# Optimization experiments

Measured on AMD Instinct MI355X. Metric: run time of the kernel, lower is better.

## Reference

```python
import jax, jax.numpy as jnp
import numpy as np

N_NODES = 100000
BN_EPS = 1e-5


def _cheb_bn_prelu(x, src, dst, w, W, b, a, g, be):
    # ChebConv K=3 with sym normalization, lambda_max=2 => L_hat = -D^-1/2 A D^-1/2
    def lap(v):
        return jax.ops.segment_sum(w[:, None] * v[src], dst, num_segments=N_NODES)
    Tx1 = lap(x)                      # [N, F]
    Tx2 = 2.0 * lap(Tx1) - x
    out = x @ W[0] + Tx1 @ W[1] + Tx2 @ W[2] + b
    out = jnp.where(out > 0, out, a * out)          # PReLU (single param)
    mu = out.mean(0)
    var = out.var(0)                                 # biased, as torch BN
    return (out - mu) / jnp.sqrt(var + BN_EPS) * g + be


def setup_inputs() -> dict:
    key = jax.random.key(0)
    ks = jax.random.split(key, 40)
    N, E, H = N_NODES, 3200000, 64
    inp = {
        'x': jax.random.normal(ks[0], (N, 3), jnp.float32),
        'pos': jax.random.normal(ks[1], (N, 3), jnp.float32),
        'normals': jax.random.normal(ks[2], (N, 3), jnp.float32),
        'edge_index': jax.random.randint(ks[3], (2, E), 0, N, jnp.int64 if jax.config.read('jax_enable_x64') else jnp.int32),
    }
    dims = [(9, H), (H, H), (H, H), (H, H // 2)]
    i = 4
    for m, (fi, fo) in enumerate(dims, start=1):
        s = 1.0 / np.sqrt(fi)
        inp[f'W{m}'] = jax.random.uniform(ks[i], (3, fi, fo), jnp.float32, -s, s); i += 1
        inp[f'b{m}'] = jax.random.uniform(ks[i], (fo,), jnp.float32, -s, s); i += 1
        inp[f'a{m}'] = jnp.full((1,), 0.25, jnp.float32)
        inp[f'g{m}'] = jnp.ones((fo,), jnp.float32)
        inp[f'be{m}'] = jnp.zeros((fo,), jnp.float32)
    hh = H // 2
    for m in range(1, 4):
        s = 1.0 / np.sqrt(hh)
        inp[f'h{m}w'] = jax.random.uniform(ks[i], (hh, hh), jnp.float32, -s, s); i += 1
        inp[f'h{m}b'] = jax.random.uniform(ks[i], (hh,), jnp.float32, -s, s); i += 1
    return inp


def reference(x, pos, normals, edge_index,
              W1, b1, a1, g1, be1, W2, b2, a2, g2, be2,
              W3, b3, a3, g3, be3, W4, b4, a4, g4, be4,
              h1w, h1b, h2w, h2b, h3w, h3b):
    src, dst = edge_index[0], edge_index[1]
    deg = jax.ops.segment_sum(jnp.ones(src.shape[0], x.dtype), src, num_segments=N_NODES)
    dis = jnp.where(deg > 0, jax.lax.rsqrt(jnp.maximum(deg, 1.0)), 0.0)
    w = -dis[src] * dis[dst]                         # scaled Laplacian edge weights
    h = jnp.concatenate([x, pos, normals], axis=1)   # [N, 9]
    h = _cheb_bn_prelu(h, src, dst, w, W1, b1, a1, g1, be1)
    h = _cheb_bn_prelu(h, src, dst, w, W2, b2, a2, g2, be2)
    h = _cheb_bn_prelu(h, src, dst, w, W3, b3, a3, g3, be3)
    h = _cheb_bn_prelu(h, src, dst, w, W4, b4, a4, g4, be4)
    h = jax.nn.relu(h @ h1w + h1b)
    h = jax.nn.relu(h @ h2w + h2b)
    return h @ h3w + h3b                              # [N, 32] logits
```

## Files before the change

kernel.cpp:

```cpp
#include <hip/hip_runtime.h>

constexpr float BN_EPS = 1e-5f;
constexpr int HB = 256;

__device__ __forceinline__ float bf2f(unsigned short u) {
  return __uint_as_float(((unsigned)u) << 16);
}
__device__ __forceinline__ unsigned short f2bf(float f) {
  union { float f; unsigned u; } v; v.f = f;
  unsigned r = v.u + 0x7FFF + ((v.u >> 16) & 1);
  return (unsigned short)(r >> 16);
}


__global__ void __launch_bounds__(1024) hist_lds_kernel(const int* __restrict__ keys, int E, int slice,
                                                        unsigned* __restrict__ partials, int NW) {
  extern __shared__ unsigned lds[];
  int tid = threadIdx.x, b = blockIdx.x;
  for (int w = tid; w < NW; w += 1024) lds[w] = 0;
  __syncthreads();
  int e0 = b * slice, e1 = e0 + slice; if (e1 > E) e1 = E;
  for (int e = e0 + tid; e < e1; e += 1024) {
    int n = keys[e];
    atomicAdd(&lds[n >> 2], 1u << (8 * (n & 3)));
  }
  __syncthreads();
  unsigned* out = partials + (size_t)b * NW;
  for (int w = tid; w < NW; w += 1024) out[w] = lds[w];
}

__global__ void combine_kernel(unsigned* __restrict__ pA, const unsigned* __restrict__ pB,
                               float* __restrict__ dis, int* __restrict__ cnt, int NW, int N) {
  int w = blockIdx.x * blockDim.x + threadIdx.x;
  if (w >= NW) return;
  unsigned sumA = 0;
  for (int b = 0; b < HB; ++b) sumA += pA[(size_t)b * NW + w];
  unsigned runB = 0;
  for (int b = 0; b < HB; ++b) {
    unsigned v = pB[(size_t)b * NW + w];
    pA[(size_t)b * NW + w] = runB;
    runB += v;
  }
  int n0 = w * 4;
#pragma unroll
  for (int j = 0; j < 4; ++j) {
    int n = n0 + j;
    if (n < N) {
      unsigned da = (sumA >> (8 * j)) & 255u;
      unsigned db = (runB >> (8 * j)) & 255u;
      dis[n] = da > 0 ? rsqrtf((float)da) : 0.f;
      cnt[n] = (int)db;
    }
  }
}

__global__ void scan1_kernel(const int* __restrict__ cnt, int N,
                             int* __restrict__ rowptr, int* __restrict__ bsums) {
  int tid = threadIdx.x, lane = tid & 63, wid = tid >> 6;
  int i = blockIdx.x * 256 + tid;
  int v = (i < N) ? cnt[i] : 0;
  int incl = v;
#pragma unroll
  for (int off = 1; off < 64; off <<= 1) {
    int u = __shfl_up(incl, off);
    if (lane >= off) incl += u;
  }
  __shared__ int wt[4];
  if (lane == 63) wt[wid] = incl;
  __syncthreads();
  int woff = 0;
  for (int w = 0; w < wid; ++w) woff += wt[w];
  if (i < N) rowptr[i] = woff + incl - v;
  if (tid == 255) bsums[blockIdx.x] = woff + incl;
}

__global__ void scan2_kernel(int* __restrict__ bsums, int NB, int* __restrict__ rowptr, int N) {
  int tid = threadIdx.x, lane = tid & 63, wid = tid >> 6;
  int v = (tid < NB) ? bsums[tid] : 0;
  int incl = v;
#pragma unroll
  for (int off = 1; off < 64; off <<= 1) {
    int u = __shfl_up(incl, off);
    if (lane >= off) incl += u;
  }
  __shared__ int wt[16];
  if (lane == 63) wt[wid] = incl;
  __syncthreads();
  int woff = 0;
  for (int w = 0; w < wid; ++w) woff += wt[w];
  if (tid < NB) bsums[tid] = woff + incl - v;
  if (tid == blockDim.x - 1) rowptr[N] = woff + incl;
}

__global__ void scan3_kernel(int* __restrict__ rowptr, const int* __restrict__ bsums, int N) {
  int i = blockIdx.x * 256 + threadIdx.x;
  if (i < N) rowptr[i] += bsums[blockIdx.x];
}

__global__ void __launch_bounds__(1024) scatter2_kernel(
    const int* __restrict__ src, const int* __restrict__ dst, int E, int slice,
    const unsigned* __restrict__ baseTbl, int NW, const int* __restrict__ rowptr,
    const float* __restrict__ dis, int2* __restrict__ pk) {
  extern __shared__ unsigned lds[];
  int tid = threadIdx.x, b = blockIdx.x;
  const unsigned* base = baseTbl + (size_t)b * NW;
  for (int w = tid; w < NW; w += 1024) lds[w] = base[w];
  __syncthreads();
  int e0 = b * slice, e1 = e0 + slice; if (e1 > E) e1 = E;
  for (int e = e0 + tid; e < e1; e += 1024) {
    int s = src[e], d = dst[e];
    unsigned prev = atomicAdd(&lds[d >> 2], 1u << (8 * (d & 3)));
    int p = rowptr[d] + (int)((prev >> (8 * (d & 3))) & 255u);
    pk[p] = make_int2(s, __float_as_int(-dis[s] * dis[d]));
  }
}

__global__ void pack_kernel(const float* __restrict__ x, const float* __restrict__ pos,
                            const float* __restrict__ nrm, ushort* __restrict__ h0b, int N) {
  int idx = blockIdx.x * blockDim.x + threadIdx.x;
  if (idx < N * 16) {
    int n = idx >> 4, c = idx & 15;
    float v = 0.f;
    if (c < 3) v = x[n * 3 + c];
    else if (c < 6) v = pos[n * 3 + c - 3];
    else if (c < 9) v = nrm[n * 3 + c - 6];
    h0b[idx] = f2bf(v);
  }
}


template <bool AFFINE>
__global__ __launch_bounds__(256) void lap64_kernel(
    const ushort4* __restrict__ vb, ushort4* __restrict__ outb,
    const int* __restrict__ rowptr, const int2* __restrict__ pk,
    const float* __restrict__ st, int N) {
  int tid = threadIdx.x, lane = tid & 63, wid = tid >> 6;
  int node = blockIdx.x * 4 + wid;
  if (node >= N) return;
  int g = lane >> 4, q = lane & 15;
  int r0 = rowptr[node], r1 = rowptr[node + 1];
  float4 a = {0.f, 0.f, 0.f, 0.f}, b = {0.f, 0.f, 0.f, 0.f};
  float ws = 0.f, ws2 = 0.f;
  int k = r0 + g;
  for (; k + 12 < r1; k += 16) {
    int2 p0 = pk[k], p1 = pk[k + 4], p2 = pk[k + 8], p3 = pk[k + 12];
    ushort4 u0 = vb[(size_t)p0.x * 16 + q];
    ushort4 u1 = vb[(size_t)p1.x * 16 + q];
    ushort4 u2 = vb[(size_t)p2.x * 16 + q];
    ushort4 u3 = vb[(size_t)p3.x * 16 + q];
    float w0 = __int_as_float(p0.y), w1 = __int_as_float(p1.y);
    float w2 = __int_as_float(p2.y), w3 = __int_as_float(p3.y);
    ws += w0 + w2; ws2 += w1 + w3;
    a.x = fmaf(w0, bf2f(u0.x), a.x); a.y = fmaf(w0, bf2f(u0.y), a.y);
    a.z = fmaf(w0, bf2f(u0.z), a.z); a.w = fmaf(w0, bf2f(u0.w), a.w);
    b.x = fmaf(w1, bf2f(u1.x), b.x); b.y = fmaf(w1, bf2f(u1.y), b.y);
    b.z = fmaf(w1, bf2f(u1.z), b.z); b.w = fmaf(w1, bf2f(u1.w), b.w);
    a.x = fmaf(w2, bf2f(u2.x), a.x); a.y = fmaf(w2, bf2f(u2.y), a.y);
    a.z = fmaf(w2, bf2f(u2.z), a.z); a.w = fmaf(w2, bf2f(u2.w), a.w);
    b.x = fmaf(w3, bf2f(u3.x), b.x); b.y = fmaf(w3, bf2f(u3.y), b.y);
    b.z = fmaf(w3, bf2f(u3.z), b.z); b.w = fmaf(w3, bf2f(u3.w), b.w);
  }
  for (; k < r1; k += 4) {
    int2 p0 = pk[k];
    ushort4 u0 = vb[(size_t)p0.x * 16 + q];
    float w0 = __int_as_float(p0.y);
    ws += w0;
    a.x = fmaf(w0, bf2f(u0.x), a.x); a.y = fmaf(w0, bf2f(u0.y), a.y);
    a.z = fmaf(w0, bf2f(u0.z), a.z); a.w = fmaf(w0, bf2f(u0.w), a.w);
  }
  a.x += b.x; a.y += b.y; a.z += b.z; a.w += b.w; ws += ws2;
  a.x += __shfl_xor(a.x, 16); a.y += __shfl_xor(a.y, 16);
  a.z += __shfl_xor(a.z, 16); a.w += __shfl_xor(a.w, 16);
  ws += __shfl_xor(ws, 16);
  a.x += __shfl_xor(a.x, 32); a.y += __shfl_xor(a.y, 32);
  a.z += __shfl_xor(a.z, 32); a.w += __shfl_xor(a.w, 32);
  ws += __shfl_xor(ws, 32);
  if (g == 0) {
    float4 o = a;
    if (AFFINE) {
      float4 s4 = *(const float4*)(st + q * 4);
      float4 t4 = *(const float4*)(st + 64 + q * 4);
      o.x = fmaf(a.x, s4.x, ws * t4.x);
      o.y = fmaf(a.y, s4.y, ws * t4.y);
      o.z = fmaf(a.z, s4.z, ws * t4.z);
      o.w = fmaf(a.w, s4.w, ws * t4.w);
    }
    ushort4 ub;
    ub.x = f2bf(o.x); ub.y = f2bf(o.y); ub.z = f2bf(o.z); ub.w = f2bf(o.w);
    outb[(size_t)node * 16 + q] = ub;
  }
}


__global__ __launch_bounds__(256) void lap16_kernel(const ushort4* __restrict__ vb,
                                                    ushort4* __restrict__ outb,
                                                    const int* __restrict__ rowptr,
                                                    const int2* __restrict__ pk, int N) {
  int tid = threadIdx.x, lane = tid & 63, wid = tid >> 6;
  int node = (blockIdx.x * 4 + wid) * 4 + (lane >> 4);
  int sub = lane & 15, g = sub >> 2, q = sub & 3;
  float4 acc = {0.f, 0.f, 0.f, 0.f};
  if (node < N) {
    int r0 = rowptr[node], r1 = rowptr[node + 1];
    for (int k = r0 + g; k < r1; k += 4) {
      int2 pr = pk[k];
      float w = __int_as_float(pr.y);
      ushort4 u = vb[(size_t)pr.x * 4 + q];
      acc.x = fmaf(w, bf2f(u.x), acc.x); acc.y = fmaf(w, bf2f(u.y), acc.y);
      acc.z = fmaf(w, bf2f(u.z), acc.z); acc.w = fmaf(w, bf2f(u.w), acc.w);
    }
  }
  acc.x += __shfl_xor(acc.x, 4); acc.y += __shfl_xor(acc.y, 4);
  acc.z += __shfl_xor(acc.z, 4); acc.w += __shfl_xor(acc.w, 4);
  acc.x += __shfl_xor(acc.x, 8); acc.y += __shfl_xor(acc.y, 8);
  acc.z += __shfl_xor(acc.z, 8); acc.w += __shfl_xor(acc.w, 8);
  if (node < N && g == 0) {
    ushort4 ub;
    ub.x = f2bf(acc.x); ub.y = f2bf(acc.y); ub.z = f2bf(acc.z); ub.w = f2bf(acc.w);
    outb[(size_t)node * 4 + q] = ub;
  }
}


template <int F_IN, int F_OUT, bool NORMH>
__global__ __launch_bounds__(256) void mm_kernel(
    const ushort* hb, const ushort* t1b, const ushort* t2b,
    ushort* outb,
    const float* __restrict__ W, const float* __restrict__ bias,
    const float* __restrict__ aP, const float* __restrict__ stPrev,
    float* __restrict__ bp, int N, int f_in_real, int ntiles) {
  constexpr int CPT = F_OUT / 16;
  constexpr int WSZ = 3 * F_IN * F_OUT;
  constexpr int RSZ = 16 * F_OUT * 2;
  constexpr int SM = (WSZ > RSZ) ? WSZ : RSZ;
  __shared__ float sm[SM];
  __shared__ float smS[F_IN], smT[F_IN];

  int tid = threadIdx.x;
  const int S = f_in_real * F_OUT;
  for (int idx = tid; idx < WSZ; idx += 256) {
    int m = idx / (F_IN * F_OUT);
    int r = idx - m * (F_IN * F_OUT);
    int i = r / F_OUT, c = r - i * F_OUT;
    float v = 0.f;
    if (i < f_in_real) {
      int b = i * F_OUT + c;
      if (m == 0)      v = W[b] - W[2 * S + b];
      else if (m == 1) v = W[S + b];
      else             v = 2.f * W[2 * S + b];
    }
    sm[idx] = v;
  }
  if (NORMH && tid < F_IN) { smS[tid] = stPrev[tid]; smT[tid] = stPrev[64 + tid]; }
  __syncthreads();

  const int cg = tid & 15;
  const int ngt = tid >> 4;
  const int c0 = cg * CPT;
  const float alpha = aP[0];
  float bb[CPT];
#pragma unroll
  for (int c = 0; c < CPT; ++c) bb[c] = bias[c0 + c];

  float ssum[CPT], ssq[CPT];
#pragma unroll
  for (int c = 0; c < CPT; ++c) { ssum[c] = 0.f; ssq[c] = 0.f; }

  for (int tile = blockIdx.x; tile < ntiles; tile += gridDim.x) {
    const int node0 = tile * 64 + ngt * 4;
    float acc[4][CPT];
#pragma unroll
    for (int j = 0; j < 4; ++j)
#pragma unroll
      for (int c = 0; c < CPT; ++c) acc[j][c] = 0.f;

#pragma unroll
    for (int m = 0; m < 3; ++m) {
      const ushort* A = (m == 0 ? hb : (m == 1 ? t1b : t2b)) + (size_t)node0 * F_IN;
      const float* Bm = sm + m * F_IN * F_OUT;
#pragma unroll 2
      for (int kb = 0; kb < F_IN / 4; ++kb) {
        float ar[4][4];
#pragma unroll
        for (int j = 0; j < 4; ++j) {
          ushort4 u = *(const ushort4*)(A + j * F_IN + kb * 4);
          ar[j][0] = bf2f(u.x); ar[j][1] = bf2f(u.y);
          ar[j][2] = bf2f(u.z); ar[j][3] = bf2f(u.w);
        }
        if (NORMH && m == 0) {
          float4 sv = *(const float4*)(smS + kb * 4);
          float4 tv = *(const float4*)(smT + kb * 4);
#pragma unroll
          for (int j = 0; j < 4; ++j) {
            ar[j][0] = fmaf(ar[j][0], sv.x, tv.x);
            ar[j][1] = fmaf(ar[j][1], sv.y, tv.y);
            ar[j][2] = fmaf(ar[j][2], sv.z, tv.z);
            ar[j][3] = fmaf(ar[j][3], sv.w, tv.w);
          }
        }
#pragma unroll
        for (int kk = 0; kk < 4; ++kk) {
          const float* Brow = Bm + (kb * 4 + kk) * F_OUT + c0;
          float br[CPT];
          if constexpr (CPT == 4) *(float4*)br = *(const float4*)Brow;
          else                    *(float2*)br = *(const float2*)Brow;
#pragma unroll
          for (int j = 0; j < 4; ++j)
#pragma unroll
            for (int c = 0; c < CPT; ++c)
              acc[j][c] = fmaf(ar[j][kk], br[c], acc[j][c]);
        }
      }
    }

#pragma unroll
    for (int j = 0; j < 4; ++j) {
      int node = node0 + j;
      if (node < N) {
        float v[CPT];
#pragma unroll
        for (int c = 0; c < CPT; ++c) {
          float t = acc[j][c] + bb[c];
          t = t > 0.f ? t : alpha * t;
          v[c] = t;
          ssum[c] += t;
          ssq[c] += t * t;
        }
        ushort* o = outb + (size_t)node * 64 + c0;
        if constexpr (CPT == 4) {
          uint2 ub;
          ub.x = (unsigned)f2bf(v[0]) | ((unsigned)f2bf(v[1]) << 16);
          ub.y = (unsigned)f2bf(v[2]) | ((unsigned)f2bf(v[3]) << 16);
          *(uint2*)o = ub;
        } else {
          unsigned ub = (unsigned)f2bf(v[0]) | ((unsigned)f2bf(v[1]) << 16);
          *(unsigned*)o = ub;
        }
      }
    }
  }

  __syncthreads();
#pragma unroll
  for (int c = 0; c < CPT; ++c) {
    sm[(ngt * F_OUT + c0 + c) * 2 + 0] = ssum[c];
    sm[(ngt * F_OUT + c0 + c) * 2 + 1] = ssq[c];
  }
  __syncthreads();
  if (tid < 128) {
    int col = tid & 63, stat = tid >> 6;
    float tot = 0.f;
    if (col < F_OUT) {
#pragma unroll 8
      for (int g = 0; g < 16; ++g) tot += sm[(g * F_OUT + col) * 2 + stat];
    }
    bp[(size_t)blockIdx.x * 128 + stat * 64 + col] = tot;
  }
}


__global__ void stats_kernel(const float* __restrict__ bp, int nb,
                             const float* __restrict__ g, const float* __restrict__ be,
                             float* __restrict__ st, int F_OUT, float invN) {
  __shared__ float red[1024];
  int tid = threadIdx.x;
  int t = tid & 127, c = tid >> 7;
  float s = 0.f;
  for (int w = c; w < nb; w += 8) s += bp[(size_t)w * 128 + t];
  red[tid] = s;
  __syncthreads();
  if (tid < 128) {
    float tot = 0.f;
    for (int cc = 0; cc < 8; ++cc) tot += red[cc * 128 + tid];
    red[tid] = tot;
  }
  __syncthreads();
  if (tid < F_OUT) {
    float sum = red[tid], sq = red[64 + tid];
    float mu = sum * invN;
    float var = sq * invN - mu * mu;
    float sc = g[tid] * rsqrtf(var + BN_EPS);
    st[tid] = sc;
    st[64 + tid] = be[tid] - mu * sc;
  }
}


__global__ __launch_bounds__(256) void mlp_kernel(const ushort* __restrict__ hb,
    const float* __restrict__ st,
    const float* __restrict__ w1, const float* __restrict__ b1,
    const float* __restrict__ w2, const float* __restrict__ b2,
    const float* __restrict__ w3, const float* __restrict__ b3,
    float* __restrict__ out, int N, int ntiles) {
  __shared__ float Wl[3][1024];
  __shared__ float Bl[3][32];
  __shared__ float S4[32], T4[32];
  __shared__ float act[2][128][36];
  int tid = threadIdx.x;
  for (int idx = tid; idx < 1024; idx += 256) {
    Wl[0][idx] = w1[idx];
    Wl[1][idx] = w2[idx];
    Wl[2][idx] = w3[idx];
  }
  if (tid < 32) {
    Bl[0][tid] = b1[tid]; Bl[1][tid] = b2[tid]; Bl[2][tid] = b3[tid];
    S4[tid] = st[tid]; T4[tid] = st[64 + tid];
  }
  __syncthreads();

  const int cg = tid & 7, ng = tid >> 3;
  const int c0 = cg * 4;
  const int nl = ng * 4;

  for (int tile = blockIdx.x; tile < ntiles; tile += gridDim.x) {
    const int node0 = tile * 128 + nl;
    float acc[4][4];

#pragma unroll
    for (int j = 0; j < 4; ++j)
#pragma unroll
      for (int c = 0; c < 4; ++c) acc[j][c] = 0.f;
#pragma unroll
    for (int kb = 0; kb < 8; ++kb) {
      float ar[4][4];
#pragma unroll
      for (int j = 0; j < 4; ++j) {
        int node = node0 + j;
        if (node < N) {
          ushort4 u = *(const ushort4*)(hb + (size_t)node * 64 + kb * 4);
          ar[j][0] = fmaf(bf2f(u.x), S4[kb * 4 + 0], T4[kb * 4 + 0]);
          ar[j][1] = fmaf(bf2f(u.y), S4[kb * 4 + 1], T4[kb * 4 + 1]);
          ar[j][2] = fmaf(bf2f(u.z), S4[kb * 4 + 2], T4[kb * 4 + 2]);
          ar[j][3] = fmaf(bf2f(u.w), S4[kb * 4 + 3], T4[kb * 4 + 3]);
        } else {
          ar[j][0] = ar[j][1] = ar[j][2] = ar[j][3] = 0.f;
        }
      }
#pragma unroll
      for (int kk = 0; kk < 4; ++kk) {
        float br[4];
        *(float4*)br = *(const float4*)(&Wl[0][(kb * 4 + kk) * 32 + c0]);
#pragma unroll
        for (int j = 0; j < 4; ++j)
#pragma unroll
          for (int c = 0; c < 4; ++c)
            acc[j][c] = fmaf(ar[j][kk], br[c], acc[j][c]);
      }
    }
#pragma unroll
    for (int j = 0; j < 4; ++j) {
      float v[4];
#pragma unroll
      for (int c = 0; c < 4; ++c) v[c] = fmaxf(acc[j][c] + Bl[0][c0 + c], 0.f);
      *(float4*)(&act[0][nl + j][c0]) = *(float4*)v;
    }
    __syncthreads();

#pragma unroll
    for (int j = 0; j < 4; ++j)
#pragma unroll
      for (int c = 0; c < 4; ++c) acc[j][c] = 0.f;
#pragma unroll
    for (int kb = 0; kb < 8; ++kb) {
      float ar[4][4];
#pragma unroll
      for (int j = 0; j < 4; ++j)
        *(float4*)ar[j] = *(const float4*)(&act[0][nl + j][kb * 4]);
#pragma unroll
      for (int kk = 0; kk < 4; ++kk) {
        float br[4];
        *(float4*)br = *(const float4*)(&Wl[1][(kb * 4 + kk) * 32 + c0]);
#pragma unroll
        for (int j = 0; j < 4; ++j)
#pragma unroll
          for (int c = 0; c < 4; ++c)
            acc[j][c] = fmaf(ar[j][kk], br[c], acc[j][c]);
      }
    }
#pragma unroll
    for (int j = 0; j < 4; ++j) {
      float v[4];
#pragma unroll
      for (int c = 0; c < 4; ++c) v[c] = fmaxf(acc[j][c] + Bl[1][c0 + c], 0.f);
      *(float4*)(&act[1][nl + j][c0]) = *(float4*)v;
    }
    __syncthreads();

#pragma unroll
    for (int j = 0; j < 4; ++j)
#pragma unroll
      for (int c = 0; c < 4; ++c) acc[j][c] = 0.f;
#pragma unroll
    for (int kb = 0; kb < 8; ++kb) {
      float ar[4][4];
#pragma unroll
      for (int j = 0; j < 4; ++j)
        *(float4*)ar[j] = *(const float4*)(&act[1][nl + j][kb * 4]);
#pragma unroll
      for (int kk = 0; kk < 4; ++kk) {
        float br[4];
        *(float4*)br = *(const float4*)(&Wl[2][(kb * 4 + kk) * 32 + c0]);
#pragma unroll
        for (int j = 0; j < 4; ++j)
#pragma unroll
          for (int c = 0; c < 4; ++c)
            acc[j][c] = fmaf(ar[j][kk], br[c], acc[j][c]);
      }
    }
#pragma unroll
    for (int j = 0; j < 4; ++j) {
      int node = node0 + j;
      if (node < N) {
        float v[4];
#pragma unroll
        for (int c = 0; c < 4; ++c) v[c] = acc[j][c] + Bl[2][c0 + c];
        *(float4*)(out + (size_t)node * 32 + c0) = *(float4*)v;
      }
    }
    __syncthreads();
  }
}


extern "C" void kernel_launch(void* const* d_in, const int* in_sizes, int n_in,
                              void* d_out, int out_size, void* d_ws, size_t ws_size,
                              hipStream_t stream) {
  const float* x   = (const float*)d_in[0];
  const float* pos = (const float*)d_in[1];
  const float* nrm = (const float*)d_in[2];
  const int*   ei  = (const int*)d_in[3];
  const float* W1p = (const float*)d_in[4];
  const float* b1p = (const float*)d_in[5];
  const float* a1p = (const float*)d_in[6];
  const float* g1p = (const float*)d_in[7];
  const float* be1p= (const float*)d_in[8];
  const float* W2p = (const float*)d_in[9];
  const float* b2p = (const float*)d_in[10];
  const float* a2p = (const float*)d_in[11];
  const float* g2p = (const float*)d_in[12];
  const float* be2p= (const float*)d_in[13];
  const float* W3p = (const float*)d_in[14];
  const float* b3p = (const float*)d_in[15];
  const float* a3p = (const float*)d_in[16];
  const float* g3p = (const float*)d_in[17];
  const float* be3p= (const float*)d_in[18];
  const float* W4p = (const float*)d_in[19];
  const float* b4p = (const float*)d_in[20];
  const float* a4p = (const float*)d_in[21];
  const float* g4p = (const float*)d_in[22];
  const float* be4p= (const float*)d_in[23];
  const float* h1w = (const float*)d_in[24];
  const float* h1b = (const float*)d_in[25];
  const float* h2w = (const float*)d_in[26];
  const float* h2b = (const float*)d_in[27];
  const float* h3w = (const float*)d_in[28];
  const float* h3b = (const float*)d_in[29];

  const int N = in_sizes[0] / 3;
  const int E = in_sizes[3] / 2;
  const int* src = ei;
  const int* dst = ei + E;

  const int NW = (N + 3) / 4;
  const size_t ldsBytes = (size_t)NW * 4;
  const int slice = (E + HB - 1) / HB;

  char* p = (char*)d_ws;
  auto alloc = [&](size_t bytes) -> void* {
    void* r = (void*)p;
    p += (bytes + 255) & ~(size_t)255;
    return r;
  };
  float*    dis      = (float*)   alloc((size_t)N * 4);
  int*      rowptr   = (int*)     alloc((size_t)(N + 1) * 4);
  int*      cnt      = (int*)     alloc((size_t)N * 4);
  int*      bsums    = (int*)     alloc(4096 * 4);
  unsigned* partialsA= (unsigned*)alloc((size_t)HB * NW * 4);
  unsigned* partialsB= (unsigned*)alloc((size_t)HB * NW * 4);
  int2*     pk       = (int2*)partialsB;
  ushort*   bufHb    = (ushort*)  alloc((size_t)N * 64 * 2);
  ushort*   bufT1b   = (ushort*)  alloc((size_t)N * 64 * 2);
  ushort*   bufT2b   = (ushort*)  alloc((size_t)N * 64 * 2);
  ushort*   bufH16b  = (ushort*)  alloc((size_t)N * 16 * 2);
  ushort*   bufT116b = (ushort*)  alloc((size_t)N * 16 * 2);
  ushort*   bufT216b = (ushort*)  alloc((size_t)N * 16 * 2);
  const int MMB = 768;
  float*    bp       = (float*)   alloc((size_t)MMB * 128 * 4);
  float*    stats    = (float*)   alloc(512 * 4);
  float* st1 = stats, *st2 = stats + 128, *st3 = stats + 256, *st4 = stats + 384;

  int gN = (N + 255) / 256;
  hist_lds_kernel<<<HB, 1024, ldsBytes, stream>>>(src, E, slice, partialsA, NW);
  hist_lds_kernel<<<HB, 1024, ldsBytes, stream>>>(dst, E, slice, partialsB, NW);
  combine_kernel<<<(NW + 255) / 256, 256, 0, stream>>>(partialsA, partialsB, dis, cnt, NW, N);
  scan1_kernel<<<gN, 256, 0, stream>>>(cnt, N, rowptr, bsums);
  scan2_kernel<<<1, 1024, 0, stream>>>(bsums, gN, rowptr, N);
  scan3_kernel<<<gN, 256, 0, stream>>>(rowptr, bsums, N);
  scatter2_kernel<<<HB, 1024, ldsBytes, stream>>>(src, dst, E, slice, partialsA, NW, rowptr, dis, pk);
  pack_kernel<<<(N * 16 + 255) / 256, 256, 0, stream>>>(x, pos, nrm, bufH16b, N);

  const float invN = 1.f / (float)N;
  int g64 = (N + 3) / 4, g16 = (N + 15) / 16;
  const int ntiles = (N + 63) / 64;
  const int ntilesM = (N + 127) / 128;

  lap16_kernel<<<g16, 256, 0, stream>>>((const ushort4*)bufH16b, (ushort4*)bufT116b, rowptr, pk, N);
  lap16_kernel<<<g16, 256, 0, stream>>>((const ushort4*)bufT116b, (ushort4*)bufT216b, rowptr, pk, N);
  mm_kernel<16, 64, false><<<MMB, 256, 0, stream>>>(bufH16b, bufT116b, bufT216b, bufHb,
      W1p, b1p, a1p, nullptr, bp, N, 9, ntiles);
  stats_kernel<<<1, 1024, 0, stream>>>(bp, MMB, g1p, be1p, st1, 64, invN);

  lap64_kernel<true><<<g64, 256, 0, stream>>>((const ushort4*)bufHb, (ushort4*)bufT1b,
      rowptr, pk, st1, N);
  lap64_kernel<false><<<g64, 256, 0, stream>>>((const ushort4*)bufT1b, (ushort4*)bufT2b,
      rowptr, pk, nullptr, N);
  mm_kernel<64, 64, true><<<MMB, 256, 0, stream>>>(bufHb, bufT1b, bufT2b, bufHb,
      W2p, b2p, a2p, st1, bp, N, 64, ntiles);
  stats_kernel<<<1, 1024, 0, stream>>>(bp, MMB, g2p, be2p, st2, 64, invN);

  lap64_kernel<true><<<g64, 256, 0, stream>>>((const ushort4*)bufHb, (ushort4*)bufT1b,
      rowptr, pk, st2, N);
  lap64_kernel<false><<<g64, 256, 0, stream>>>((const ushort4*)bufT1b, (ushort4*)bufT2b,
      rowptr, pk, nullptr, N);
  mm_kernel<64, 64, true><<<MMB, 256, 0, stream>>>(bufHb, bufT1b, bufT2b, bufHb,
      W3p, b3p, a3p, st2, bp, N, 64, ntiles);
  stats_kernel<<<1, 1024, 0, stream>>>(bp, MMB, g3p, be3p, st3, 64, invN);

  lap64_kernel<true><<<g64, 256, 0, stream>>>((const ushort4*)bufHb, (ushort4*)bufT1b,
      rowptr, pk, st3, N);
  lap64_kernel<false><<<g64, 256, 0, stream>>>((const ushort4*)bufT1b, (ushort4*)bufT2b,
      rowptr, pk, nullptr, N);
  mm_kernel<64, 32, true><<<MMB, 256, 0, stream>>>(bufHb, bufT1b, bufT2b, bufHb,
      W4p, b4p, a4p, st3, bp, N, 64, ntiles);
  stats_kernel<<<1, 1024, 0, stream>>>(bp, MMB, g4p, be4p, st4, 32, invN);

  mlp_kernel<<<MMB, 256, 0, stream>>>(bufHb, st4, h1w, h1b, h2w, h2b, h3w, h3b,
      (float*)d_out, N, ntilesM);
}
```

Baseline: 908.4 us.

## Replace scalar FMA dense transforms with bf16 MFMA kernel and fold BN into weights

The per-layer dense transform (three Chebyshev terms times weight matrices) moves from scalar fp32 FMAs to 16x16x32 bf16 MFMA instructions, with weight fragments held in registers. The previous layer's batch-norm scale is folded into the weights and its shift into the bias, so the per-element normalization in the inner loop goes away. The first layer packs x, T1 and T2 into one 64-wide interleaved buffer so it runs as a single K=64 MFMA pass. Weights are now rounded to bf16, which adds precision error, and the wider first-layer buffer adds some memory traffic.

```diff
diff --git a/kernel.cpp b/kernel.cpp
--- a/kernel.cpp
+++ b/kernel.cpp
@@ -2,6 +2,9 @@
 
 constexpr float BN_EPS = 1e-5f;
 constexpr int HB = 256;
+
+using short8  = __attribute__((ext_vector_type(8))) short;
+using floatx4 = __attribute__((ext_vector_type(4))) float;
 
 __device__ __forceinline__ float bf2f(unsigned short u) {
   return __uint_as_float(((unsigned)u) << 16);
@@ -116,15 +119,15 @@
 }
 
 __global__ void pack_kernel(const float* __restrict__ x, const float* __restrict__ pos,
-                            const float* __restrict__ nrm, ushort* __restrict__ h0b, int N) {
+                            const float* __restrict__ nrm, ushort* __restrict__ h0c, int N) {
   int idx = blockIdx.x * blockDim.x + threadIdx.x;
-  if (idx < N * 16) {
-    int n = idx >> 4, c = idx & 15;
+  if (idx < N * 64) {
+    int n = idx >> 6, c = idx & 63;
     float v = 0.f;
     if (c < 3) v = x[n * 3 + c];
     else if (c < 6) v = pos[n * 3 + c - 3];
     else if (c < 9) v = nrm[n * 3 + c - 6];
-    h0b[idx] = f2bf(v);
+    h0c[idx] = f2bf(v);
   }
 }
 
@@ -195,7 +198,8 @@
 __global__ __launch_bounds__(256) void lap16_kernel(const ushort4* __restrict__ vb,
                                                     ushort4* __restrict__ outb,
                                                     const int* __restrict__ rowptr,
-                                                    const int2* __restrict__ pk, int N) {
+                                                    const int2* __restrict__ pk, int N,
+                                                    int inOff, int outOff) {
   int tid = threadIdx.x, lane = tid & 63, wid = tid >> 6;
   int node = (blockIdx.x * 4 + wid) * 4 + (lane >> 4);
   int sub = lane & 15, g = sub >> 2, q = sub & 3;
@@ -205,7 +209,7 @@
     for (int k = r0 + g; k < r1; k += 4) {
       int2 pr = pk[k];
       float w = __int_as_float(pr.y);
-      ushort4 u = vb[(size_t)pr.x * 4 + q];
+      ushort4 u = vb[(size_t)pr.x * 16 + inOff + q];
       acc.x = fmaf(w, bf2f(u.x), acc.x); acc.y = fmaf(w, bf2f(u.y), acc.y);
       acc.z = fmaf(w, bf2f(u.z), acc.z); acc.w = fmaf(w, bf2f(u.w), acc.w);
     }
@@ -217,143 +221,127 @@
   if (node < N && g == 0) {
     ushort4 ub;
     ub.x = f2bf(acc.x); ub.y = f2bf(acc.y); ub.z = f2bf(acc.z); ub.w = f2bf(acc.w);
-    outb[(size_t)node * 4 + q] = ub;
-  }
-}
-
-
-template <int F_IN, int F_OUT, bool NORMH>
-__global__ __launch_bounds__(256) void mm_kernel(
-    const ushort* hb, const ushort* t1b, const ushort* t2b,
-    ushort* outb,
+    outb[(size_t)node * 16 + outOff + q] = ub;
+  }
+}
+
+
+template <int NMAT, int F_OUT, bool NORMH>
+__global__ __launch_bounds__(256) void mmfma_kernel(
+    const ushort* __restrict__ A0, const ushort* __restrict__ A1, const ushort* __restrict__ A2,
+    ushort* __restrict__ outb,
     const float* __restrict__ W, const float* __restrict__ bias,
     const float* __restrict__ aP, const float* __restrict__ stPrev,
     float* __restrict__ bp, int N, int f_in_real, int ntiles) {
-  constexpr int CPT = F_OUT / 16;
-  constexpr int WSZ = 3 * F_IN * F_OUT;
-  constexpr int RSZ = 16 * F_OUT * 2;
-  constexpr int SM = (WSZ > RSZ) ? WSZ : RSZ;
-  __shared__ float sm[SM];
-  __shared__ float smS[F_IN], smT[F_IN];
-
+  constexpr int NFRAG = F_OUT / 16;
+  constexpr int NKF = NMAT * 2;
+  constexpr int TOTF = NKF * NFRAG;
+  __shared__ ushort fragW[TOTF * 512];
+  __shared__ float biasL[64];
+  __shared__ float red[4 * 2 * 64];
   int tid = threadIdx.x;
+
   const int S = f_in_real * F_OUT;
-  for (int idx = tid; idx < WSZ; idx += 256) {
-    int m = idx / (F_IN * F_OUT);
-    int r = idx - m * (F_IN * F_OUT);
-    int i = r / F_OUT, c = r - i * F_OUT;
+  for (int idx = tid; idx < TOTF * 512; idx += 256) {
+    int f = idx >> 9;
+    int r = idx & 511;
+    int l = r >> 3, j = r & 7;
+    int kf = f / NFRAG, nc = f - kf * NFRAG;
+    int c = nc * 16 + (l & 15);
     float v = 0.f;
-    if (i < f_in_real) {
-      int b = i * F_OUT + c;
-      if (m == 0)      v = W[b] - W[2 * S + b];
-      else if (m == 1) v = W[S + b];
-      else             v = 2.f * W[2 * S + b];
-    }
-    sm[idx] = v;
-  }
-  if (NORMH && tid < F_IN) { smS[tid] = stPrev[tid]; smT[tid] = stPrev[64 + tid]; }
-  __syncthreads();
-
-  const int cg = tid & 15;
-  const int ngt = tid >> 4;
-  const int c0 = cg * CPT;
+    if (NMAT == 3) {
+      int k = (kf & 1) * 32 + (l >> 4) * 8 + j;
+      int m = kf >> 1;
+      int b = k * F_OUT + c;
+      if (m == 0)      { v = W[b] - W[2 * S + b]; if (NORMH) v *= stPrev[k]; }
+      else if (m == 1)   v = W[S + b];
+      else               v = 2.f * W[2 * S + b];
+    } else {
+      int kg = kf * 32 + (l >> 4) * 8 + j;
+      int sub = kg >> 4, kk = kg & 15;
+      if (sub < 3 && kk < f_in_real) {
+        int b = kk * F_OUT + c;
+        if (sub == 0)      v = W[b] - W[2 * S + b];
+        else if (sub == 1) v = W[S + b];
+        else               v = 2.f * W[2 * S + b];
+      }
+    }
+    fragW[idx] = f2bf(v);
+  }
+  if (tid < F_OUT) {
+    float acc = bias[tid];
+    if (NORMH) {
+      for (int k = 0; k < 64; ++k)
+        acc += stPrev[64 + k] * (W[k * F_OUT + tid] - W[2 * S + k * F_OUT + tid]);
+    }
+    biasL[tid] = acc;
+  }
+  for (int idx = tid; idx < 512; idx += 256) red[idx] = 0.f;
+  __syncthreads();
+
+  const int lane = tid & 63, wid = tid >> 6;
+  const int rg = lane >> 4, cl = lane & 15;
   const float alpha = aP[0];
-  float bb[CPT];
-#pragma unroll
-  for (int c = 0; c < CPT; ++c) bb[c] = bias[c0 + c];
-
-  float ssum[CPT], ssq[CPT];
-#pragma unroll
-  for (int c = 0; c < CPT; ++c) { ssum[c] = 0.f; ssq[c] = 0.f; }
+
+  short8 bfr[TOTF];
+#pragma unroll
+  for (int f = 0; f < TOTF; ++f)
+    bfr[f] = *(const short8*)&fragW[f * 512 + lane * 8];
+
+  float ssum[NFRAG], ssq[NFRAG];
+#pragma unroll
+  for (int nc = 0; nc < NFRAG; ++nc) { ssum[nc] = 0.f; ssq[nc] = 0.f; }
 
   for (int tile = blockIdx.x; tile < ntiles; tile += gridDim.x) {
-    const int node0 = tile * 64 + ngt * 4;
-    float acc[4][CPT];
-#pragma unroll
-    for (int j = 0; j < 4; ++j)
-#pragma unroll
-      for (int c = 0; c < CPT; ++c) acc[j][c] = 0.f;
-
-#pragma unroll
-    for (int m = 0; m < 3; ++m) {
-      const ushort* A = (m == 0 ? hb : (m == 1 ? t1b : t2b)) + (size_t)node0 * F_IN;
-      const float* Bm = sm + m * F_IN * F_OUT;
-#pragma unroll 2
-      for (int kb = 0; kb < F_IN / 4; ++kb) {
-        float ar[4][4];
-#pragma unroll
-        for (int j = 0; j < 4; ++j) {
-          ushort4 u = *(const ushort4*)(A + j * F_IN + kb * 4);
-          ar[j][0] = bf2f(u.x); ar[j][1] = bf2f(u.y);
-          ar[j][2] = bf2f(u.z); ar[j][3] = bf2f(u.w);
-        }
-        if (NORMH && m == 0) {
-          float4 sv = *(const float4*)(smS + kb * 4);
-          float4 tv = *(const float4*)(smT + kb * 4);
-#pragma unroll
-          for (int j = 0; j < 4; ++j) {
-            ar[j][0] = fmaf(ar[j][0], sv.x, tv.x);
-            ar[j][1] = fmaf(ar[j][1], sv.y, tv.y);
-            ar[j][2] = fmaf(ar[j][2], sv.z, tv.z);
-            ar[j][3] = fmaf(ar[j][3], sv.w, tv.w);
-          }
-        }
-#pragma unroll
-        for (int kk = 0; kk < 4; ++kk) {
-          const float* Brow = Bm + (kb * 4 + kk) * F_OUT + c0;
-          float br[CPT];
-          if constexpr (CPT == 4) *(float4*)br = *(const float4*)Brow;
-          else                    *(float2*)br = *(const float2*)Brow;
-#pragma unroll
-          for (int j = 0; j < 4; ++j)
-#pragma unroll
-            for (int c = 0; c < CPT; ++c)
-              acc[j][c] = fmaf(ar[j][kk], br[c], acc[j][c]);
+    const int nb = tile * 64 + wid * 16;
+    floatx4 acc[NFRAG];
+#pragma unroll
+    for (int nc = 0; nc < NFRAG; ++nc) acc[nc] = (floatx4){0.f, 0.f, 0.f, 0.f};
+
+#pragma unroll
+    for (int kf = 0; kf < NKF; ++kf) {
+      const ushort* Ap = (NMAT == 1) ? A0 : (kf < 2 ? A0 : (kf < 4 ? A1 : A2));
+      int kc = kf & 1;
+      short8 a = *(const short8*)(Ap + (size_t)(nb + cl) * 64 + kc * 32 + rg * 8);
+#pragma unroll
+      for (int nc = 0; nc < NFRAG; ++nc)
+        acc[nc] = __builtin_amdgcn_mfma_f32_16x16x32_bf16(a, bfr[kf * NFRAG + nc], acc[nc], 0, 0, 0);
+    }
+
+#pragma unroll
+    for (int nc = 0; nc < NFRAG; ++nc) {
+      int c = nc * 16 + cl;
+      float bi = biasL[c];
+#pragma unroll
+      for (int r = 0; r < 4; ++r) {
+        int node = nb + rg * 4 + r;
+        if (node < N) {
+          float t = acc[nc][r] + bi;
+          t = t > 0.f ? t : alpha * t;
+          ssum[nc] += t; ssq[nc] += t * t;
+          outb[(size_t)node * 64 + c] = f2bf(t);
         }
       }
     }
-
-#pragma unroll
-    for (int j = 0; j < 4; ++j) {
-      int node = node0 + j;
-      if (node < N) {
-        float v[CPT];
-#pragma unroll
-        for (int c = 0; c < CPT; ++c) {
-          float t = acc[j][c] + bb[c];
-          t = t > 0.f ? t : alpha * t;
-          v[c] = t;
-          ssum[c] += t;
-          ssq[c] += t * t;
-        }
-        ushort* o = outb + (size_t)node * 64 + c0;
-        if constexpr (CPT == 4) {
-          uint2 ub;
-          ub.x = (unsigned)f2bf(v[0]) | ((unsigned)f2bf(v[1]) << 16);
-          ub.y = (unsigned)f2bf(v[2]) | ((unsigned)f2bf(v[3]) << 16);
-          *(uint2*)o = ub;
-        } else {
-          unsigned ub = (unsigned)f2bf(v[0]) | ((unsigned)f2bf(v[1]) << 16);
-          *(unsigned*)o = ub;
-        }
-      }
-    }
-  }
-
-  __syncthreads();
-#pragma unroll
-  for (int c = 0; c < CPT; ++c) {
-    sm[(ngt * F_OUT + c0 + c) * 2 + 0] = ssum[c];
-    sm[(ngt * F_OUT + c0 + c) * 2 + 1] = ssq[c];
+  }
+
+#pragma unroll
+  for (int nc = 0; nc < NFRAG; ++nc) {
+    ssum[nc] += __shfl_xor(ssum[nc], 16); ssum[nc] += __shfl_xor(ssum[nc], 32);
+    ssq[nc]  += __shfl_xor(ssq[nc], 16);  ssq[nc]  += __shfl_xor(ssq[nc], 32);
+  }
+  if (lane < 16) {
+#pragma unroll
+    for (int nc = 0; nc < NFRAG; ++nc) {
+      red[(wid * 2 + 0) * 64 + nc * 16 + lane] = ssum[nc];
+      red[(wid * 2 + 1) * 64 + nc * 16 + lane] = ssq[nc];
+    }
   }
   __syncthreads();
   if (tid < 128) {
     int col = tid & 63, stat = tid >> 6;
-    float tot = 0.f;
-    if (col < F_OUT) {
-#pragma unroll 8
-      for (int g = 0; g < 16; ++g) tot += sm[(g * F_OUT + col) * 2 + stat];
-    }
+    float tot = red[(0 * 2 + stat) * 64 + col] + red[(1 * 2 + stat) * 64 + col]
+              + red[(2 * 2 + stat) * 64 + col] + red[(3 * 2 + stat) * 64 + col];
     bp[(size_t)blockIdx.x * 128 + stat * 64 + col] = tot;
   }
 }
@@ -581,9 +569,7 @@
   ushort*   bufHb    = (ushort*)  alloc((size_t)N * 64 * 2);
   ushort*   bufT1b   = (ushort*)  alloc((size_t)N * 64 * 2);
   ushort*   bufT2b   = (ushort*)  alloc((size_t)N * 64 * 2);
-  ushort*   bufH16b  = (ushort*)  alloc((size_t)N * 16 * 2);
-  ushort*   bufT116b = (ushort*)  alloc((size_t)N * 16 * 2);
-  ushort*   bufT216b = (ushort*)  alloc((size_t)N * 16 * 2);
+  ushort*   bufC16   = (ushort*)  alloc((size_t)N * 64 * 2);
   const int MMB = 768;
   float*    bp       = (float*)   alloc((size_t)MMB * 128 * 4);
   float*    stats    = (float*)   alloc(512 * 4);
@@ -597,16 +583,16 @@
   scan2_kernel<<<1, 1024, 0, stream>>>(bsums, gN, rowptr, N);
   scan3_kernel<<<gN, 256, 0, stream>>>(rowptr, bsums, N);
   scatter2_kernel<<<HB, 1024, ldsBytes, stream>>>(src, dst, E, slice, partialsA, NW, rowptr, dis, pk);
-  pack_kernel<<<(N * 16 + 255) / 256, 256, 0, stream>>>(x, pos, nrm, bufH16b, N);
+  pack_kernel<<<(N * 64 + 255) / 256, 256, 0, stream>>>(x, pos, nrm, bufC16, N);
 
   const float invN = 1.f / (float)N;
   int g64 = (N + 3) / 4, g16 = (N + 15) / 16;
   const int ntiles = (N + 63) / 64;
   const int ntilesM = (N + 127) / 128;
 
-  lap16_kernel<<<g16, 256, 0, stream>>>((const ushort4*)bufH16b, (ushort4*)bufT116b, rowptr, pk, N);
-  lap16_kernel<<<g16, 256, 0, stream>>>((const ushort4*)bufT116b, (ushort4*)bufT216b, rowptr, pk, N);
-  mm_kernel<16, 64, false><<<MMB, 256, 0, stream>>>(bufH16b, bufT116b, bufT216b, bufHb,
+  lap16_kernel<<<g16, 256, 0, stream>>>((const ushort4*)bufC16, (ushort4*)bufC16, rowptr, pk, N, 0, 4);
+  lap16_kernel<<<g16, 256, 0, stream>>>((const ushort4*)bufC16, (ushort4*)bufC16, rowptr, pk, N, 4, 8);
+  mmfma_kernel<1, 64, false><<<MMB, 256, 0, stream>>>(bufC16, nullptr, nullptr, bufHb,
       W1p, b1p, a1p, nullptr, bp, N, 9, ntiles);
   stats_kernel<<<1, 1024, 0, stream>>>(bp, MMB, g1p, be1p, st1, 64, invN);
 
@@ -614,7 +600,7 @@
       rowptr, pk, st1, N);
   lap64_kernel<false><<<g64, 256, 0, stream>>>((const ushort4*)bufT1b, (ushort4*)bufT2b,
       rowptr, pk, nullptr, N);
-  mm_kernel<64, 64, true><<<MMB, 256, 0, stream>>>(bufHb, bufT1b, bufT2b, bufHb,
+  mmfma_kernel<3, 64, true><<<MMB, 256, 0, stream>>>(bufHb, bufT1b, bufT2b, bufHb,
       W2p, b2p, a2p, st1, bp, N, 64, ntiles);
   stats_kernel<<<1, 1024, 0, stream>>>(bp, MMB, g2p, be2p, st2, 64, invN);
 
@@ -622,7 +608,7 @@
       rowptr, pk, st2, N);
   lap64_kernel<false><<<g64, 256, 0, stream>>>((const ushort4*)bufT1b, (ushort4*)bufT2b,
       rowptr, pk, nullptr, N);
-  mm_kernel<64, 64, true><<<MMB, 256, 0, stream>>>(bufHb, bufT1b, bufT2b, bufHb,
+  mmfma_kernel<3, 64, true><<<MMB, 256, 0, stream>>>(bufHb, bufT1b, bufT2b, bufHb,
       W3p, b3p, a3p, st2, bp, N, 64, ntiles);
   stats_kernel<<<1, 1024, 0, stream>>>(bp, MMB, g3p, be3p, st3, 64, invN);
 
@@ -630,7 +616,7 @@
       rowptr, pk, st3, N);
   lap64_kernel<false><<<g64, 256, 0, stream>>>((const ushort4*)bufT1b, (ushort4*)bufT2b,
       rowptr, pk, nullptr, N);
-  mm_kernel<64, 32, true><<<MMB, 256, 0, stream>>>(bufHb, bufT1b, bufT2b, bufHb,
+  mmfma_kernel<3, 32, true><<<MMB, 256, 0, stream>>>(bufHb, bufT1b, bufT2b, bufHb,
       W4p, b4p, a4p, st3, bp, N, 64, ntiles);
   stats_kernel<<<1, 1024, 0, stream>>>(bp, MMB, g4p, be4p, st4, 32, invN);
 
```

After: 864.8 us. 4.8% less time.
